# Kernel optimization log

Measured on AMD Instinct MI355X. Metric: run time of the kernel, lower is better.

Reference implementation:

```python
import jax, jax.numpy as jnp
import numpy as np


def setup_inputs() -> dict:
    key = jax.random.key(0)
    k1, k2 = jax.random.split(key)
    B, T, H = 4096, 50, 512
    query = jax.random.normal(k1, (B, H), dtype=jnp.float32)
    utterances = jax.random.normal(k2, (T, B, H), dtype=jnp.float32)
    return {"query": query, "utterances": utterances}


def reference(query, utterances):
    # query: [B, H]; utterances: [T, B, H]
    # cosine similarity between query and each utterance
    p = jnp.einsum("bh,tbh->bt", query, utterances)          # [B, T]
    q_norm = jnp.linalg.norm(query, axis=1, keepdims=True)    # [B, 1]
    u_norm = jnp.linalg.norm(utterances, axis=2).T            # [B, T]
    p = p / q_norm / u_norm
    # append fixed score 1 for the query itself, then softmax over T+1
    ones = jnp.ones((p.shape[0], 1), dtype=p.dtype)
    p = jax.nn.softmax(jnp.concatenate([p, ones], axis=1), axis=1)  # [B, T+1]
    # weighted sum over [utterances; query]
    utt_b = jnp.transpose(utterances, (1, 0, 2))              # [B, T, H]
    vector = jnp.concatenate([utt_b, query[:, None, :]], axis=1)  # [B, T+1, H]
    return jnp.einsum("bt,bth->bh", p, vector)                # [B, H]
```

## Files before the change

### kernel.cpp

```cpp
#include <hip/hip_runtime.h>
#include <math.h>

#define T_UTT 50
#define H_DIM 512
#define B_DIM 4096
#define NWAVES 8
#define NT_PW 7

typedef float f32x4 __attribute__((ext_vector_type(4)));

__device__ __forceinline__ float dot8(f32x4 a0, f32x4 a1, f32x4 b0, f32x4 b1) {
    float s = 0.f;
#pragma unroll
    for (int j = 0; j < 4; ++j) s += a0[j] * b0[j];
#pragma unroll
    for (int j = 0; j < 4; ++j) s += a1[j] * b1[j];
    return s;
}

__global__ __launch_bounds__(512, 4) void wseq_attn(const float* __restrict__ Q,
                                                    const float* __restrict__ U,
                                                    float* __restrict__ Out) {
    const int b    = blockIdx.x;
    const int tid  = threadIdx.x;
    const int lane = tid & 63;
    const int wave = tid >> 6;
    const int h0   = lane << 3;

    __shared__ float s_score[T_UTT];
    __shared__ float s_q[H_DIM];
    __shared__ float s_part[NWAVES][H_DIM];

    const f32x4* qp = reinterpret_cast<const f32x4*>(Q + (size_t)b * H_DIM + h0);
    f32x4 q0 = qp[0];
    f32x4 q1 = qp[1];

    f32x4 u0[NT_PW], u1[NT_PW];
#pragma unroll
    for (int i = 0; i < NT_PW; ++i) {
        const int t = wave + NWAVES * i;
        if (t < T_UTT) {
            const f32x4* up =
                reinterpret_cast<const f32x4*>(U + ((size_t)t * B_DIM + b) * H_DIM + h0);
            u0[i] = __builtin_nontemporal_load(up);
            u1[i] = __builtin_nontemporal_load(up + 1);
        }
    }

    if (wave == 0) {
        *reinterpret_cast<f32x4*>(&s_q[h0])     = q0;
        *reinterpret_cast<f32x4*>(&s_q[h0 + 4]) = q1;
    }

    float qn = dot8(q0, q1, q0, q1);
#pragma unroll
    for (int m = 32; m; m >>= 1) qn += __shfl_xor(qn, m, 64);
    const float q_inv = rsqrtf(qn);

#pragma unroll
    for (int i = 0; i < NT_PW; ++i) {
        const int t = wave + NWAVES * i;
        if (t < T_UTT) {
            float d = dot8(q0, q1, u0[i], u1[i]);
            float n = dot8(u0[i], u1[i], u0[i], u1[i]);
#pragma unroll
            for (int m = 32; m; m >>= 1) {
                d += __shfl_xor(d, m, 64);
                n += __shfl_xor(n, m, 64);
            }
            if (lane == 0) s_score[t] = d * q_inv * rsqrtf(n);
        }
    }
    __syncthreads();

    float v = (lane < T_UTT) ? s_score[lane]
                             : ((lane == T_UTT) ? 1.0f : -INFINITY);
    float mx = v;
#pragma unroll
    for (int m = 32; m; m >>= 1) mx = fmaxf(mx, __shfl_xor(mx, m, 64));
    float e = __expf(v - mx);
    float sum = e;
#pragma unroll
    for (int m = 32; m; m >>= 1) sum += __shfl_xor(sum, m, 64);
    const float ew = e * (1.0f / sum);

    float acc[8] = {0.f, 0.f, 0.f, 0.f, 0.f, 0.f, 0.f, 0.f};
#pragma unroll
    for (int i = 0; i < NT_PW; ++i) {
        const int t = wave + NWAVES * i;
        if (t < T_UTT) {
            const float w = __shfl(ew, t, 64);
            acc[0] += w * u0[i][0]; acc[1] += w * u0[i][1];
            acc[2] += w * u0[i][2]; acc[3] += w * u0[i][3];
            acc[4] += w * u1[i][0]; acc[5] += w * u1[i][1];
            acc[6] += w * u1[i][2]; acc[7] += w * u1[i][3];
        }
    }
    f32x4* sp = reinterpret_cast<f32x4*>(&s_part[wave][h0]);
    sp[0] = (f32x4){acc[0], acc[1], acc[2], acc[3]};
    sp[1] = (f32x4){acc[4], acc[5], acc[6], acc[7]};
    __syncthreads();

    const float wq = __shfl(ew, T_UTT, 64);
    float o = wq * s_q[tid];
#pragma unroll
    for (int w = 0; w < NWAVES; ++w) o += s_part[w][tid];
    __builtin_nontemporal_store(o, &Out[(size_t)b * H_DIM + tid]);
}

extern "C" void kernel_launch(void* const* d_in, const int* in_sizes, int n_in,
                              void* d_out, int out_size, void* d_ws, size_t ws_size,
                              hipStream_t stream) {
    const float* Q = (const float*)d_in[0];
    const float* U = (const float*)d_in[1];
    float* Out = (float*)d_out;
    wseq_attn<<<dim3(B_DIM), dim3(512), 0, stream>>>(Q, U, Out);
}
```

Baseline: 93.72 us.

## Use persistent 1024-thread blocks with double-buffered register prefetch across batch rows

Result: slower. 105.0 us (+12.1%).

```diff
diff --git a/kernel.cpp b/kernel.cpp
--- a/kernel.cpp
+++ b/kernel.cpp
@@ -4,8 +4,10 @@
 #define T_UTT 50
 #define H_DIM 512
 #define B_DIM 4096
-#define NWAVES 8
-#define NT_PW 7
+#define NWAVES 16
+#define NT_PW 4
+#define NBLK 256
+#define GENS 16
 
 typedef float f32x4 __attribute__((ext_vector_type(4)));
 
@@ -18,94 +20,123 @@
     return s;
 }
 
-__global__ __launch_bounds__(512, 4) void wseq_attn(const float* __restrict__ Q,
-                                                    const float* __restrict__ U,
-                                                    float* __restrict__ Out) {
-    const int b    = blockIdx.x;
+#define STEP(cu0, cu1, cq0, cq1, nu0, nu1, nq0, nq1, g)                          \
+    {                                                                            \
+             \
+        if ((g) + 1 < GENS) {                                                    \
+            const int bn = ((g) + 1) * NBLK + k;                                 \
+            const f32x4* qp = reinterpret_cast<const f32x4*>(                    \
+                Q + (size_t)bn * H_DIM + h0);                                    \
+            nq0 = qp[0]; nq1 = qp[1];                                            \
+            _Pragma("unroll")                                                    \
+            for (int i = 0; i < NT_PW; ++i) {                                    \
+                const int t = wave + NWAVES * i;                                 \
+                if (t < T_UTT) {                                                 \
+                    const f32x4* up = reinterpret_cast<const f32x4*>(            \
+                        U + ((size_t)t * B_DIM + bn) * H_DIM + h0);              \
+                    nu0[i] = up[0]; nu1[i] = up[1];                              \
+                }                                                                \
+            }                                                                    \
+        }                                                                        \
+                                           \
+        _Pragma("unroll")                                                        \
+        for (int i = 0; i < NT_PW; ++i) {                                        \
+            const int t = wave + NWAVES * i;                                     \
+            if (t < T_UTT) {                                                     \
+                float d = dot8(cq0, cq1, cu0[i], cu1[i]);                        \
+                float n = dot8(cu0[i], cu1[i], cu0[i], cu1[i]);                  \
+                _Pragma("unroll")                                                \
+                for (int m = 32; m; m >>= 1) {                                   \
+                    d += __shfl_xor(d, m, 64);                                   \
+                    n += __shfl_xor(n, m, 64);                                   \
+                }                                                                \
+                if (lane == 0) s_score[t] = d * rsqrtf(n);                       \
+            }                                                                    \
+        }                                                                        \
+        __syncthreads();                                                  \
+        if (wave == 0) {                                                         \
+            float qn = dot8(cq0, cq1, cq0, cq1);                                 \
+            _Pragma("unroll")                                                    \
+            for (int m = 32; m; m >>= 1) qn += __shfl_xor(qn, m, 64);            \
+            const float q_inv = rsqrtf(qn);                                      \
+            *reinterpret_cast<f32x4*>(&s_q[h0])     = cq0;                       \
+            *reinterpret_cast<f32x4*>(&s_q[h0 + 4]) = cq1;                       \
+            float v = (lane < T_UTT) ? s_score[lane] * q_inv                     \
+                                     : ((lane == T_UTT) ? 1.0f : -INFINITY);     \
+            float mx = v;                                                        \
+            _Pragma("unroll")                                                    \
+            for (int m = 32; m; m >>= 1) mx = fmaxf(mx, __shfl_xor(mx, m, 64));  \
+            float e = __expf(v - mx);                                            \
+            float sum = e;                                                       \
+            _Pragma("unroll")                                                    \
+            for (int m = 32; m; m >>= 1) sum += __shfl_xor(sum, m, 64);          \
+            if (lane <= T_UTT) s_w[lane] = e / sum;                              \
+        }                                                                        \
+        __syncthreads();                                                  \
+        {                                                                        \
+            float acc[8] = {0.f, 0.f, 0.f, 0.f, 0.f, 0.f, 0.f, 0.f};             \
+            _Pragma("unroll")                                                    \
+            for (int i = 0; i < NT_PW; ++i) {                                    \
+                const int t = wave + NWAVES * i;                                 \
+                if (t < T_UTT) {                                                 \
+                    const float w = s_w[t];                                      \
+                    acc[0] += w * cu0[i][0]; acc[1] += w * cu0[i][1];            \
+                    acc[2] += w * cu0[i][2]; acc[3] += w * cu0[i][3];            \
+                    acc[4] += w * cu1[i][0]; acc[5] += w * cu1[i][1];            \
+                    acc[6] += w * cu1[i][2]; acc[7] += w * cu1[i][3];            \
+                }                                                                \
+            }                                                                    \
+            f32x4* sp = reinterpret_cast<f32x4*>(&s_part[wave][h0]);             \
+            sp[0] = (f32x4){acc[0], acc[1], acc[2], acc[3]};                     \
+            sp[1] = (f32x4){acc[4], acc[5], acc[6], acc[7]};                     \
+        }                                                                        \
+        __syncthreads();                                                  \
+        if (tid < H_DIM) {                                                       \
+            float o = s_w[T_UTT] * s_q[tid];                                     \
+            _Pragma("unroll")                                                    \
+            for (int w = 0; w < NWAVES; ++w) o += s_part[w][tid];                \
+            Out[(size_t)((g) * NBLK + k) * H_DIM + tid] = o;                     \
+        }                                                                        \
+    }
+
+__global__ __launch_bounds__(1024, 4) void wseq_attn(const float* __restrict__ Q,
+                                                     const float* __restrict__ U,
+                                                     float* __restrict__ Out) {
+    const int k0   = blockIdx.x;
+    const int k    = (k0 & 7) * (NBLK / 8) + (k0 >> 3);
     const int tid  = threadIdx.x;
     const int lane = tid & 63;
     const int wave = tid >> 6;
     const int h0   = lane << 3;
 
     __shared__ float s_score[T_UTT];
+    __shared__ float s_w[T_UTT + 1];
     __shared__ float s_q[H_DIM];
     __shared__ float s_part[NWAVES][H_DIM];
 
-    const f32x4* qp = reinterpret_cast<const f32x4*>(Q + (size_t)b * H_DIM + h0);
-    f32x4 q0 = qp[0];
-    f32x4 q1 = qp[1];
+    f32x4 uA0[NT_PW], uA1[NT_PW], qA0, qA1;
+    f32x4 uB0[NT_PW], uB1[NT_PW], qB0, qB1;
 
-    f32x4 u0[NT_PW], u1[NT_PW];
+    {
+        const int b = k;
+        const f32x4* qp = reinterpret_cast<const f32x4*>(Q + (size_t)b * H_DIM + h0);
+        qA0 = qp[0]; qA1 = qp[1];
 #pragma unroll
-    for (int i = 0; i < NT_PW; ++i) {
-        const int t = wave + NWAVES * i;
-        if (t < T_UTT) {
-            const f32x4* up =
-                reinterpret_cast<const f32x4*>(U + ((size_t)t * B_DIM + b) * H_DIM + h0);
-            u0[i] = __builtin_nontemporal_load(up);
-            u1[i] = __builtin_nontemporal_load(up + 1);
+        for (int i = 0; i < NT_PW; ++i) {
+            const int t = wave + NWAVES * i;
+            if (t < T_UTT) {
+                const f32x4* up = reinterpret_cast<const f32x4*>(
+                    U + ((size_t)t * B_DIM + b) * H_DIM + h0);
+                uA0[i] = up[0]; uA1[i] = up[1];
+            }
         }
     }
 
-    if (wave == 0) {
-        *reinterpret_cast<f32x4*>(&s_q[h0])     = q0;
-        *reinterpret_cast<f32x4*>(&s_q[h0 + 4]) = q1;
+#pragma unroll 1
+    for (int g = 0; g < GENS; g += 2) {
+        STEP(uA0, uA1, qA0, qA1, uB0, uB1, qB0, qB1, g);
+        STEP(uB0, uB1, qB0, qB1, uA0, uA1, qA0, qA1, g + 1);
     }
-
-    float qn = dot8(q0, q1, q0, q1);
-#pragma unroll
-    for (int m = 32; m; m >>= 1) qn += __shfl_xor(qn, m, 64);
-    const float q_inv = rsqrtf(qn);
-
-#pragma unroll
-    for (int i = 0; i < NT_PW; ++i) {
-        const int t = wave + NWAVES * i;
-        if (t < T_UTT) {
-            float d = dot8(q0, q1, u0[i], u1[i]);
-            float n = dot8(u0[i], u1[i], u0[i], u1[i]);
-#pragma unroll
-            for (int m = 32; m; m >>= 1) {
-                d += __shfl_xor(d, m, 64);
-                n += __shfl_xor(n, m, 64);
-            }
-            if (lane == 0) s_score[t] = d * q_inv * rsqrtf(n);
-        }
-    }
-    __syncthreads();
-
-    float v = (lane < T_UTT) ? s_score[lane]
-                             : ((lane == T_UTT) ? 1.0f : -INFINITY);
-    float mx = v;
-#pragma unroll
-    for (int m = 32; m; m >>= 1) mx = fmaxf(mx, __shfl_xor(mx, m, 64));
-    float e = __expf(v - mx);
-    float sum = e;
-#pragma unroll
-    for (int m = 32; m; m >>= 1) sum += __shfl_xor(sum, m, 64);
-    const float ew = e * (1.0f / sum);
-
-    float acc[8] = {0.f, 0.f, 0.f, 0.f, 0.f, 0.f, 0.f, 0.f};
-#pragma unroll
-    for (int i = 0; i < NT_PW; ++i) {
-        const int t = wave + NWAVES * i;
-        if (t < T_UTT) {
-            const float w = __shfl(ew, t, 64);
-            acc[0] += w * u0[i][0]; acc[1] += w * u0[i][1];
-            acc[2] += w * u0[i][2]; acc[3] += w * u0[i][3];
-            acc[4] += w * u1[i][0]; acc[5] += w * u1[i][1];
-            acc[6] += w * u1[i][2]; acc[7] += w * u1[i][3];
-        }
-    }
-    f32x4* sp = reinterpret_cast<f32x4*>(&s_part[wave][h0]);
-    sp[0] = (f32x4){acc[0], acc[1], acc[2], acc[3]};
-    sp[1] = (f32x4){acc[4], acc[5], acc[6], acc[7]};
-    __syncthreads();
-
-    const float wq = __shfl(ew, T_UTT, 64);
-    float o = wq * s_q[tid];
-#pragma unroll
-    for (int w = 0; w < NWAVES; ++w) o += s_part[w][tid];
-    __builtin_nontemporal_store(o, &Out[(size_t)b * H_DIM + tid]);
 }
 
 extern "C" void kernel_launch(void* const* d_in, const int* in_sizes, int n_in,
@@ -114,5 +145,5 @@
     const float* Q = (const float*)d_in[0];
     const float* U = (const float*)d_in[1];
     float* Out = (float*)d_out;
-    wseq_attn<<<dim3(B_DIM), dim3(512), 0, stream>>>(Q, U, Out);
+    wseq_attn<<<dim3(NBLK), dim3(1024), 0, stream>>>(Q, U, Out);
 }
```

## Stream utterances per 32-lane group with fixed-max online softmax and double buffering

Applied to the files above, without the earlier changes.

Result: faster. 76.75 us (-18.1%).

```diff
diff --git a/kernel.cpp b/kernel.cpp
--- a/kernel.cpp
+++ b/kernel.cpp
@@ -4,108 +4,95 @@
 #define T_UTT 50
 #define H_DIM 512
 #define B_DIM 4096
-#define NWAVES 8
-#define NT_PW 7
+#define GRP 32
+#define NB 8
+#define NFL 4
 
 typedef float f32x4 __attribute__((ext_vector_type(4)));
 
-__device__ __forceinline__ float dot8(f32x4 a0, f32x4 a1, f32x4 b0, f32x4 b1) {
-    float s = 0.f;
-#pragma unroll
-    for (int j = 0; j < 4; ++j) s += a0[j] * b0[j];
-#pragma unroll
-    for (int j = 0; j < 4; ++j) s += a1[j] * b1[j];
-    return s;
-}
+#define COMPUTE(u)                                                      \
+    {                                                                   \
+        float d = 0.f, n = 0.f;                                         \
+        _Pragma("unroll")                                               \
+        for (int j = 0; j < NFL; ++j) {                                 \
+            _Pragma("unroll")                                           \
+            for (int c = 0; c < 4; ++c) {                               \
+                d += q[j][c] * u[j][c];                                 \
+                n += u[j][c] * u[j][c];                                 \
+            }                                                           \
+        }                                                               \
+        _Pragma("unroll")                                               \
+        for (int m = 16; m; m >>= 1) {                                  \
+            d += __shfl_xor(d, m, GRP);                                 \
+            n += __shfl_xor(n, m, GRP);                                 \
+        }                                                               \
+        const float e = __expf(d * rsqrtf(n) * q_inv - 1.0f);           \
+        lsum += e;                                                      \
+        _Pragma("unroll")                                               \
+        for (int j = 0; j < NFL; ++j) {                                 \
+            _Pragma("unroll")                                           \
+            for (int c = 0; c < 4; ++c) acc[j][c] += e * u[j][c];       \
+        }                                                               \
+    }
 
-__global__ __launch_bounds__(512, 4) void wseq_attn(const float* __restrict__ Q,
+__global__ __launch_bounds__(256, 4) void wseq_attn(const float* __restrict__ Q,
                                                     const float* __restrict__ U,
                                                     float* __restrict__ Out) {
-    const int b    = blockIdx.x;
-    const int tid  = threadIdx.x;
-    const int lane = tid & 63;
-    const int wave = tid >> 6;
-    const int h0   = lane << 3;
+    const int tid = threadIdx.x;
+    const int g   = tid & (GRP - 1);
+    const int bl  = tid >> 5;
+    const int b   = blockIdx.x * NB + bl;
 
-    __shared__ float s_score[T_UTT];
-    __shared__ float s_q[H_DIM];
-    __shared__ float s_part[NWAVES][H_DIM];
+    const f32x4* qp = reinterpret_cast<const f32x4*>(Q + (size_t)b * H_DIM) + g;
+    f32x4 q[NFL];
+#pragma unroll
+    for (int j = 0; j < NFL; ++j) q[j] = qp[j * GRP];
 
-    const f32x4* qp = reinterpret_cast<const f32x4*>(Q + (size_t)b * H_DIM + h0);
-    f32x4 q0 = qp[0];
-    f32x4 q1 = qp[1];
+    float qn = 0.f;
+#pragma unroll
+    for (int j = 0; j < NFL; ++j)
+        qn += q[j][0]*q[j][0] + q[j][1]*q[j][1] + q[j][2]*q[j][2] + q[j][3]*q[j][3];
+#pragma unroll
+    for (int m = 16; m; m >>= 1) qn += __shfl_xor(qn, m, GRP);
+    const float q_inv = rsqrtf(qn);
 
-    f32x4 u0[NT_PW], u1[NT_PW];
+    const f32x4*  ub      = reinterpret_cast<const f32x4*>(U + (size_t)b * H_DIM) + g;
+    const size_t  tstride = (size_t)B_DIM * H_DIM / 4;
+
+    f32x4 acc[NFL];
 #pragma unroll
-    for (int i = 0; i < NT_PW; ++i) {
-        const int t = wave + NWAVES * i;
-        if (t < T_UTT) {
-            const f32x4* up =
-                reinterpret_cast<const f32x4*>(U + ((size_t)t * B_DIM + b) * H_DIM + h0);
-            u0[i] = __builtin_nontemporal_load(up);
-            u1[i] = __builtin_nontemporal_load(up + 1);
+    for (int j = 0; j < NFL; ++j) acc[j] = (f32x4){0.f, 0.f, 0.f, 0.f};
+    float lsum = 0.f;
+
+    f32x4 uA[NFL], uB[NFL];
+#pragma unroll
+    for (int j = 0; j < NFL; ++j) uA[j] = ub[j * GRP];
+
+#pragma unroll 1
+    for (int t = 0; t < T_UTT; t += 2) {
+        {
+            const f32x4* p = ub + (size_t)(t + 1) * tstride;
+#pragma unroll
+            for (int j = 0; j < NFL; ++j) uB[j] = p[j * GRP];
         }
+        COMPUTE(uA);
+        if (t + 2 < T_UTT) {
+            const f32x4* p = ub + (size_t)(t + 2) * tstride;
+#pragma unroll
+            for (int j = 0; j < NFL; ++j) uA[j] = p[j * GRP];
+        }
+        COMPUTE(uB);
     }
 
-    if (wave == 0) {
-        *reinterpret_cast<f32x4*>(&s_q[h0])     = q0;
-        *reinterpret_cast<f32x4*>(&s_q[h0 + 4]) = q1;
+    const float inv_l = 1.0f / (lsum + 1.0f);
+    f32x4* op = reinterpret_cast<f32x4*>(Out + (size_t)b * H_DIM) + g;
+#pragma unroll
+    for (int j = 0; j < NFL; ++j) {
+        f32x4 o;
+#pragma unroll
+        for (int c = 0; c < 4; ++c) o[c] = (acc[j][c] + q[j][c]) * inv_l;
+        op[j * GRP] = o;
     }
-
-    float qn = dot8(q0, q1, q0, q1);
-#pragma unroll
-    for (int m = 32; m; m >>= 1) qn += __shfl_xor(qn, m, 64);
-    const float q_inv = rsqrtf(qn);
-
-#pragma unroll
-    for (int i = 0; i < NT_PW; ++i) {
-        const int t = wave + NWAVES * i;
-        if (t < T_UTT) {
-            float d = dot8(q0, q1, u0[i], u1[i]);
-            float n = dot8(u0[i], u1[i], u0[i], u1[i]);
-#pragma unroll
-            for (int m = 32; m; m >>= 1) {
-                d += __shfl_xor(d, m, 64);
-                n += __shfl_xor(n, m, 64);
-            }
-            if (lane == 0) s_score[t] = d * q_inv * rsqrtf(n);
-        }
-    }
-    __syncthreads();
-
-    float v = (lane < T_UTT) ? s_score[lane]
-                             : ((lane == T_UTT) ? 1.0f : -INFINITY);
-    float mx = v;
-#pragma unroll
-    for (int m = 32; m; m >>= 1) mx = fmaxf(mx, __shfl_xor(mx, m, 64));
-    float e = __expf(v - mx);
-    float sum = e;
-#pragma unroll
-    for (int m = 32; m; m >>= 1) sum += __shfl_xor(sum, m, 64);
-    const float ew = e * (1.0f / sum);
-
-    float acc[8] = {0.f, 0.f, 0.f, 0.f, 0.f, 0.f, 0.f, 0.f};
-#pragma unroll
-    for (int i = 0; i < NT_PW; ++i) {
-        const int t = wave + NWAVES * i;
-        if (t < T_UTT) {
-            const float w = __shfl(ew, t, 64);
-            acc[0] += w * u0[i][0]; acc[1] += w * u0[i][1];
-            acc[2] += w * u0[i][2]; acc[3] += w * u0[i][3];
-            acc[4] += w * u1[i][0]; acc[5] += w * u1[i][1];
-            acc[6] += w * u1[i][2]; acc[7] += w * u1[i][3];
-        }
-    }
-    f32x4* sp = reinterpret_cast<f32x4*>(&s_part[wave][h0]);
-    sp[0] = (f32x4){acc[0], acc[1], acc[2], acc[3]};
-    sp[1] = (f32x4){acc[4], acc[5], acc[6], acc[7]};
-    __syncthreads();
-
-    const float wq = __shfl(ew, T_UTT, 64);
-    float o = wq * s_q[tid];
-#pragma unroll
-    for (int w = 0; w < NWAVES; ++w) o += s_part[w][tid];
-    __builtin_nontemporal_store(o, &Out[(size_t)b * H_DIM + tid]);
 }
 
 extern "C" void kernel_launch(void* const* d_in, const int* in_sizes, int n_in,
@@ -114,5 +101,5 @@
     const float* Q = (const float*)d_in[0];
     const float* U = (const float*)d_in[1];
     float* Out = (float*)d_out;
-    wseq_attn<<<dim3(B_DIM), dim3(512), 0, stream>>>(Q, U, Out);
+    wseq_attn<<<dim3(B_DIM / NB), dim3(256), 0, stream>>>(Q, U, Out);
 }
```
